# Performance work log

Measured on AMD Instinct MI355X. Metric: run time of the kernel, lower is better.

Reference implementation:

```python
import jax, jax.numpy as jnp
import numpy as np

B, N, D, H = 2, 64, 256, 8
DK = D // H
EPS = 1e-5


def layer_norm(x, g, b):
    mu = jnp.mean(x, axis=-1, keepdims=True)
    var = jnp.var(x, axis=-1, keepdims=True)
    return (x - mu) * jax.lax.rsqrt(var + EPS) * g + b


def setup_inputs() -> dict:
    key = jax.random.key(0)
    ks = jax.random.split(key, 12)
    s = 1.0 / np.sqrt(D)
    inp = {
        "x": jax.random.normal(ks[0], (B, N, N, D), jnp.float32),
        "W_lk": jax.random.uniform(ks[1], (D, D), jnp.float32, -s, s),
        "W_rk": jax.random.uniform(ks[2], (D, D), jnp.float32, -s, s),
        "W_lv": jax.random.uniform(ks[3], (D, D), jnp.float32, -s, s),
        "W_rv": jax.random.uniform(ks[4], (D, D), jnp.float32, -s, s),
        "W_out": jax.random.uniform(ks[5], (D, D), jnp.float32, -s, s),
        "ln_agg_g": jnp.ones((D,), jnp.float32),
        "ln_agg_b": jnp.zeros((D,), jnp.float32),
        "W1": jax.random.uniform(ks[6], (D, 2 * D), jnp.float32, -s, s),
        "b1": jnp.zeros((2 * D,), jnp.float32),
        "W2": jax.random.uniform(ks[7], (2 * D, D), jnp.float32, -1.0 / np.sqrt(2 * D), 1.0 / np.sqrt(2 * D)),
        "b2": jnp.zeros((D,), jnp.float32),
        "ln2_g": jnp.ones((D,), jnp.float32),
        "ln2_b": jnp.zeros((D,), jnp.float32),
    }
    return inp


def reference(x, W_lk, W_rk, W_lv, W_rv, W_out, ln_agg_g, ln_agg_b, W1, b1, W2, b2, ln2_g, ln2_b):
    b, n = x.shape[0], x.shape[1]
    # projections (no bias), split into heads: [b, n, n, H, DK]
    lk = (x @ W_lk).reshape(b, n, n, H, DK)
    rk = (x @ W_rk).reshape(b, n, n, H, DK)
    lv = (x @ W_lv).reshape(b, n, n, H, DK)
    rv = (x @ W_rv).reshape(b, n, n, H, DK)
    # triangle attention scores over intermediate node 'a'
    scores = jnp.einsum('bxahd,bayhd->bxayh', lk, rk) / np.sqrt(DK)
    att = jax.nn.softmax(scores, axis=2)
    # fused triangle value aggregation: sum_a att * lv[x,a] * rv[a,y]
    o = jnp.einsum('bxayh,bxahd,bayhd->bxyhd', att, lv, rv)
    o = o.reshape(b, n, n, D) @ W_out
    # FFN block (dropout = 0)
    h = layer_norm(x + o, ln_agg_g, ln_agg_b)
    m = jax.nn.relu(h @ W1 + b1) @ W2 + b2
    return layer_norm(m + h, ln2_g, ln2_b)
```

## Files before the change

kernel.cpp:

```cpp
#include <hip/hip_runtime.h>

#define ROWS 8192
#define DIM  256

typedef short short8 __attribute__((ext_vector_type(8)));
typedef float f4     __attribute__((ext_vector_type(4)));

__device__ __forceinline__ float bf2f(unsigned int u16) {
    union { unsigned int i; float f; } v;
    v.i = (u16 & 0xffffu) << 16;
    return v.f;
}
__device__ __forceinline__ unsigned short f2bf(float f) {
    union { float f; unsigned int u; } v; v.f = f;
    unsigned int r = v.u + 0x7fffu + ((v.u >> 16) & 1u);
    return (unsigned short)(r >> 16);
}

__global__ __launch_bounds__(256)
void cast_all(const float* __restrict__ x, unsigned short* __restrict__ xb,
              const float* __restrict__ w0, const float* __restrict__ w1,
              const float* __restrict__ w2, const float* __restrict__ w3,
              const float* __restrict__ w4, const float* __restrict__ w5,
              const float* __restrict__ w6, unsigned short* __restrict__ wt)
{
    if (blockIdx.x < 2048) {
        const size_t i = ((size_t)blockIdx.x * 256 + threadIdx.x) * 4;
        float4 v = *(const float4*)(x + i);
        uint2 p;
        p.x = f2bf(v.x) | ((unsigned int)f2bf(v.y) << 16);
        p.y = f2bf(v.z) | ((unsigned int)f2bf(v.w) << 16);
        *(uint2*)(xb + i) = p;
        return;
    }
    __shared__ float t[32][33];
    int id = blockIdx.x - 2048;
    const float* src; int K, N, Ntiles; size_t doff;
    if (id < 320) {
        int w = id >> 6; id &= 63; K = 256; N = 256; Ntiles = 8;
        doff = (size_t)w * 65536;
        src = (w == 0) ? w0 : (w == 1) ? w1 : (w == 2) ? w2 : (w == 3) ? w3 : w4;
    } else if (id < 448) {
        id -= 320; K = 256; N = 512; Ntiles = 16; doff = 327680; src = w5;
    } else {
        id -= 448; K = 512; N = 256; Ntiles = 8;  doff = 458752; src = w6;
    }
    const int tk = id / Ntiles, tn = id % Ntiles;
    const int k0 = tk * 32, n0 = tn * 32;
    const int c = threadIdx.x & 31, r8 = threadIdx.x >> 5;
    for (int rr = r8; rr < 32; rr += 8)
        t[rr][c] = src[(size_t)(k0 + rr) * N + n0 + c];
    __syncthreads();
    for (int rr = r8; rr < 32; rr += 8)
        wt[doff + (size_t)(n0 + rr) * K + k0 + c] = f2bf(t[c][rr]);
}

__global__ __launch_bounds__(256)
void proj_mfma(const unsigned short* __restrict__ A, const unsigned short* __restrict__ WT,
               unsigned short* __restrict__ projT)
{
    const int lane = threadIdx.x & 63, wave = threadIdx.x >> 6;
    const int wsel = blockIdx.x >> 2;
    const int col0 = (blockIdx.x & 3) * 64;
    const int m0 = blockIdx.y * 128 + wave * 32;
    const int lm = lane & 15, lk8 = (lane >> 4) * 8;
    const unsigned short* W = WT + (size_t)wsel * 65536;
    unsigned short* dst = projT + (size_t)wsel * 2097152;

    f4 acc[2][4];
    #pragma unroll
    for (int i = 0; i < 2; ++i)
        #pragma unroll
        for (int j = 0; j < 4; ++j) acc[i][j] = (f4){0.f, 0.f, 0.f, 0.f};

    #pragma unroll 2
    for (int kc = 0; kc < 256; kc += 32) {
        short8 af[2], bf[4];
        #pragma unroll
        for (int i = 0; i < 2; ++i)
            af[i] = *(const short8*)(A + (size_t)(m0 + i * 16 + lm) * 256 + kc + lk8);
        #pragma unroll
        for (int j = 0; j < 4; ++j)
            bf[j] = *(const short8*)(W + (size_t)(col0 + j * 16 + lm) * 256 + kc + lk8);
        #pragma unroll
        for (int i = 0; i < 2; ++i)
            #pragma unroll
            for (int j = 0; j < 4; ++j)
                acc[i][j] = __builtin_amdgcn_mfma_f32_16x16x32_bf16(af[i], bf[j], acc[i][j], 0, 0, 0);
    }

    const int rbase = (lane >> 4) * 4;
    const int swap = (wsel == 3);
    #pragma unroll
    for (int i = 0; i < 2; ++i)
        #pragma unroll
        for (int j = 0; j < 4; ++j) {
            const int c = col0 + j * 16 + lm;
            const int h = c >> 5, d = c & 31;
            #pragma unroll
            for (int r = 0; r < 4; ++r) {
                const int m = m0 + i * 16 + rbase + r;
                const int b = m >> 12, ii = (m >> 6) & 63, jj = m & 63;
                const int p = swap ? jj : ii;
                const int q = swap ? ii : jj;
                const size_t idx = ((((size_t)b * 8 + h) * 64 + p) * 64 + q) * 32 + d;
                dst[idx] = f2bf(acc[i][j][r]);
            }
        }
}

__global__ __launch_bounds__(256)
void scores_mfma(const unsigned short* __restrict__ lkT, const unsigned short* __restrict__ rkT,
                 unsigned short* __restrict__ S)
{
    const int lane = threadIdx.x & 63, wave = threadIdx.x >> 6;
    const int bi = blockIdx.x;
    const int b = bi >> 7, h = (bi >> 4) & 7, a = (bi & 15) * 4 + wave;
    const size_t bh = (size_t)b * 8 + h;
    const int lm = lane & 15, lk8 = (lane >> 4) * 8;

    short8 af[4], bf[4];
    #pragma unroll
    for (int t = 0; t < 4; ++t) {
        af[t] = *(const short8*)(lkT + ((bh * 64 + (t * 16 + lm)) * 64 + a) * 32 + lk8);
        bf[t] = *(const short8*)(rkT + ((bh * 64 + a) * 64 + (t * 16 + lm)) * 32 + lk8);
    }
    const int rbase = (lane >> 4) * 4;
    unsigned short* Sb = S + bh * 262144 + a * 64;
    #pragma unroll
    for (int mt = 0; mt < 4; ++mt)
        #pragma unroll
        for (int nt = 0; nt < 4; ++nt) {
            f4 acc = (f4){0.f, 0.f, 0.f, 0.f};
            acc = __builtin_amdgcn_mfma_f32_16x16x32_bf16(af[mt], bf[nt], acc, 0, 0, 0);
            #pragma unroll
            for (int r = 0; r < 4; ++r) {
                const int xx = mt * 16 + rbase + r;
                const int yy = nt * 16 + lm;
                Sb[(size_t)xx * 4096 + yy] = f2bf(acc[r] * 0.17677669529663687f);
            }
        }
}

__global__ __launch_bounds__(256)
void softmax_agg(const unsigned short* __restrict__ S, const unsigned short* __restrict__ lvT,
                 const unsigned short* __restrict__ rvT, unsigned short* __restrict__ obuf)
{
    __shared__ float att[64][64];
    __shared__ float lvL[64][32];
    __shared__ float smx[4][64], ssm[4][64], invL[64];
    const int bi = blockIdx.x;
    const int b = bi >> 9, h = (bi >> 6) & 7, x = bi & 63;
    const size_t bh = (size_t)b * 8 + h;
    const int tid = threadIdx.x;

    {
        const int a = tid >> 2, yo = (tid & 3) * 16;
        const unsigned short* Sp = S + (bh * 64 + x) * 4096 + a * 64 + yo;
        uint4 p0 = *(const uint4*)(Sp);
        uint4 p1 = *(const uint4*)(Sp + 8);
        att[a][yo +  0] = bf2f(p0.x); att[a][yo +  1] = bf2f(p0.x >> 16);
        att[a][yo +  2] = bf2f(p0.y); att[a][yo +  3] = bf2f(p0.y >> 16);
        att[a][yo +  4] = bf2f(p0.z); att[a][yo +  5] = bf2f(p0.z >> 16);
        att[a][yo +  6] = bf2f(p0.w); att[a][yo +  7] = bf2f(p0.w >> 16);
        att[a][yo +  8] = bf2f(p1.x); att[a][yo +  9] = bf2f(p1.x >> 16);
        att[a][yo + 10] = bf2f(p1.y); att[a][yo + 11] = bf2f(p1.y >> 16);
        att[a][yo + 12] = bf2f(p1.z); att[a][yo + 13] = bf2f(p1.z >> 16);
        att[a][yo + 14] = bf2f(p1.w); att[a][yo + 15] = bf2f(p1.w >> 16);
        const int d0 = (tid & 3) * 8;
        uint4 q = *(const uint4*)(lvT + ((bh * 64 + x) * 64 + a) * 32 + d0);
        lvL[a][d0 + 0] = bf2f(q.x); lvL[a][d0 + 1] = bf2f(q.x >> 16);
        lvL[a][d0 + 2] = bf2f(q.y); lvL[a][d0 + 3] = bf2f(q.y >> 16);
        lvL[a][d0 + 4] = bf2f(q.z); lvL[a][d0 + 5] = bf2f(q.z >> 16);
        lvL[a][d0 + 6] = bf2f(q.w); lvL[a][d0 + 7] = bf2f(q.w >> 16);
    }
    __syncthreads();

    {
        const int y = tid & 63, az = tid >> 6;
        float mx = -1e30f;
        for (int a = az; a < 64; a += 4) mx = fmaxf(mx, att[a][y]);
        smx[az][y] = mx;
    }
    __syncthreads();

    {
        const int y = tid & 63, az = tid >> 6;
        const float mx = fmaxf(fmaxf(smx[0][y], smx[1][y]), fmaxf(smx[2][y], smx[3][y]));
        float s = 0.f;
        for (int a = az; a < 64; a += 4) {
            float e = __expf(att[a][y] - mx);
            att[a][y] = e;
            s += e;
        }
        ssm[az][y] = s;
    }
    __syncthreads();
    if (tid < 64)
        invL[tid] = 1.f / (ssm[0][tid] + ssm[1][tid] + ssm[2][tid] + ssm[3][tid]);
    __syncthreads();

    {
        const int y = tid >> 2, d0 = (tid & 3) * 8;
        float o[8];
        #pragma unroll
        for (int i = 0; i < 8; ++i) o[i] = 0.f;
        const unsigned short* rvr = rvT + (bh * 64 + y) * 2048 + d0;
        #pragma unroll 8
        for (int a = 0; a < 64; ++a) {
            const float w = att[a][y];
            float4 lv0 = *(const float4*)&lvL[a][d0];
            float4 lv1 = *(const float4*)&lvL[a][d0 + 4];
            uint4 rv4 = *(const uint4*)(rvr + (size_t)a * 32);
            o[0] = fmaf(w * lv0.x, bf2f(rv4.x),       o[0]);
            o[1] = fmaf(w * lv0.y, bf2f(rv4.x >> 16), o[1]);
            o[2] = fmaf(w * lv0.z, bf2f(rv4.y),       o[2]);
            o[3] = fmaf(w * lv0.w, bf2f(rv4.y >> 16), o[3]);
            o[4] = fmaf(w * lv1.x, bf2f(rv4.z),       o[4]);
            o[5] = fmaf(w * lv1.y, bf2f(rv4.z >> 16), o[5]);
            o[6] = fmaf(w * lv1.z, bf2f(rv4.w),       o[6]);
            o[7] = fmaf(w * lv1.w, bf2f(rv4.w >> 16), o[7]);
        }
        const float inv = invL[y];
        uint4 pk;
        pk.x = f2bf(o[0] * inv) | ((unsigned int)f2bf(o[1] * inv) << 16);
        pk.y = f2bf(o[2] * inv) | ((unsigned int)f2bf(o[3] * inv) << 16);
        pk.z = f2bf(o[4] * inv) | ((unsigned int)f2bf(o[5] * inv) << 16);
        pk.w = f2bf(o[6] * inv) | ((unsigned int)f2bf(o[7] * inv) << 16);
        *(uint4*)(obuf + (((size_t)b * 64 + x) * 64 + y) * 256 + h * 32 + d0) = pk;
    }
}

__global__ __launch_bounds__(256)
void gemm_ln1(const unsigned short* __restrict__ A, const unsigned short* __restrict__ WT,
              const float* __restrict__ resid,
              const float* __restrict__ gamma, const float* __restrict__ beta,
              unsigned short* __restrict__ out)
{
    constexpr int K = 256;
    __shared__ float ps[16][4], pq[16][4];
    const int lane = threadIdx.x & 63, wave = threadIdx.x >> 6;
    const int m0 = blockIdx.x * 16;
    const int col0 = wave * 64;
    const int lm = lane & 15, lk8 = (lane >> 4) * 8;

    f4 acc[4];
    #pragma unroll
    for (int j = 0; j < 4; ++j) acc[j] = (f4){0.f, 0.f, 0.f, 0.f};

    #pragma unroll 2
    for (int kc = 0; kc < K; kc += 32) {
        short8 af = *(const short8*)(A + (size_t)(m0 + lm) * K + kc + lk8);
        #pragma unroll
        for (int j = 0; j < 4; ++j) {
            short8 bf = *(const short8*)(WT + (size_t)(col0 + j * 16 + lm) * K + kc + lk8);
            acc[j] = __builtin_amdgcn_mfma_f32_16x16x32_bf16(af, bf, acc[j], 0, 0, 0);
        }
    }

    const int rbase = (lane >> 4) * 4;
    float v[4][4];
    float s[4] = {0.f, 0.f, 0.f, 0.f}, q[4] = {0.f, 0.f, 0.f, 0.f};
    #pragma unroll
    for (int j = 0; j < 4; ++j) {
        const int n = col0 + j * 16 + lm;
        #pragma unroll
        for (int r = 0; r < 4; ++r) {
            const int m = m0 + rbase + r;
            float t = acc[j][r] + resid[(size_t)m * 256 + n];
            v[j][r] = t;
            s[r] += t;
            q[r] = fmaf(t, t, q[r]);
        }
    }
    #pragma unroll
    for (int off = 1; off < 16; off <<= 1) {
        #pragma unroll
        for (int r = 0; r < 4; ++r) {
            s[r] += __shfl_xor(s[r], off);
            q[r] += __shfl_xor(q[r], off);
        }
    }
    if (lm == 0) {
        #pragma unroll
        for (int r = 0; r < 4; ++r) {
            ps[rbase + r][wave] = s[r];
            pq[rbase + r][wave] = q[r];
        }
    }
    __syncthreads();
    #pragma unroll
    for (int r = 0; r < 4; ++r) {
        const int lr = rbase + r;
        const float Sm = ps[lr][0] + ps[lr][1] + ps[lr][2] + ps[lr][3];
        const float Qm = pq[lr][0] + pq[lr][1] + pq[lr][2] + pq[lr][3];
        const float mu = Sm * (1.f / 256.f);
        const float ri = rsqrtf(Qm * (1.f / 256.f) - mu * mu + 1e-5f);
        const int m = m0 + lr;
        #pragma unroll
        for (int j = 0; j < 4; ++j) {
            const int n = col0 + j * 16 + lm;
            out[(size_t)m * 256 + n] = f2bf((v[j][r] - mu) * ri * gamma[n] + beta[n]);
        }
    }
}

__global__ __launch_bounds__(256)
void ffn_fused(const unsigned short* __restrict__ hb, const unsigned short* __restrict__ WT1,
               const float* __restrict__ b1, const unsigned short* __restrict__ WT2,
               const float* __restrict__ b2, const float* __restrict__ gamma,
               const float* __restrict__ beta, float* __restrict__ out)
{
    __shared__ unsigned short mid[16][520];
    __shared__ float ps[16][4], pq[16][4];
    const int lane = threadIdx.x & 63, wave = threadIdx.x >> 6;
    const int m0 = blockIdx.x * 16;
    const int lm = lane & 15, lk8 = (lane >> 4) * 8;
    const int rbase = (lane >> 4) * 4;

    short8 af[8];
    #pragma unroll
    for (int kc = 0; kc < 8; ++kc)
        af[kc] = *(const short8*)(hb + (size_t)(m0 + lm) * 256 + kc * 32 + lk8);
    const int colb = wave * 128;
    #pragma unroll
    for (int j = 0; j < 8; ++j) {
        const int n = colb + j * 16 + lm;
        f4 acc = (f4){0.f, 0.f, 0.f, 0.f};
        #pragma unroll
        for (int kc = 0; kc < 8; ++kc) {
            short8 bf = *(const short8*)(WT1 + (size_t)n * 256 + kc * 32 + lk8);
            acc = __builtin_amdgcn_mfma_f32_16x16x32_bf16(af[kc], bf, acc, 0, 0, 0);
        }
        const float bb = b1[n];
        #pragma unroll
        for (int r = 0; r < 4; ++r)
            mid[rbase + r][n] = f2bf(fmaxf(acc[r] + bb, 0.f));
    }
    __syncthreads();

    const int col0 = wave * 64;
    f4 acc2[4];
    #pragma unroll
    for (int j = 0; j < 4; ++j) acc2[j] = (f4){0.f, 0.f, 0.f, 0.f};
    #pragma unroll 4
    for (int kc = 0; kc < 16; ++kc) {
        short8 a2 = *(const short8*)&mid[lm][kc * 32 + lk8];
        #pragma unroll
        for (int j = 0; j < 4; ++j) {
            short8 bf = *(const short8*)(WT2 + (size_t)(col0 + j * 16 + lm) * 512 + kc * 32 + lk8);
            acc2[j] = __builtin_amdgcn_mfma_f32_16x16x32_bf16(a2, bf, acc2[j], 0, 0, 0);
        }
    }

    float v[4][4];
    float s[4] = {0.f, 0.f, 0.f, 0.f}, q[4] = {0.f, 0.f, 0.f, 0.f};
    #pragma unroll
    for (int j = 0; j < 4; ++j) {
        const int n = col0 + j * 16 + lm;
        const float bb = b2[n];
        #pragma unroll
        for (int r = 0; r < 4; ++r) {
            const int m = m0 + rbase + r;
            float t = acc2[j][r] + bb + bf2f(hb[(size_t)m * 256 + n]);
            v[j][r] = t;
            s[r] += t;
            q[r] = fmaf(t, t, q[r]);
        }
    }
    #pragma unroll
    for (int off = 1; off < 16; off <<= 1) {
        #pragma unroll
        for (int r = 0; r < 4; ++r) {
            s[r] += __shfl_xor(s[r], off);
            q[r] += __shfl_xor(q[r], off);
        }
    }
    if (lm == 0) {
        #pragma unroll
        for (int r = 0; r < 4; ++r) {
            ps[rbase + r][wave] = s[r];
            pq[rbase + r][wave] = q[r];
        }
    }
    __syncthreads();
    #pragma unroll
    for (int r = 0; r < 4; ++r) {
        const int lr = rbase + r;
        const float Sm = ps[lr][0] + ps[lr][1] + ps[lr][2] + ps[lr][3];
        const float Qm = pq[lr][0] + pq[lr][1] + pq[lr][2] + pq[lr][3];
        const float mu = Sm * (1.f / 256.f);
        const float ri = rsqrtf(Qm * (1.f / 256.f) - mu * mu + 1e-5f);
        const int m = m0 + lr;
        #pragma unroll
        for (int j = 0; j < 4; ++j) {
            const int n = col0 + j * 16 + lm;
            out[(size_t)m * 256 + n] = (v[j][r] - mu) * ri * gamma[n] + beta[n];
        }
    }
}

extern "C" void kernel_launch(void* const* d_in, const int* in_sizes, int n_in,
                              void* d_out, int out_size, void* d_ws, size_t ws_size,
                              hipStream_t stream)
{
    const float* x    = (const float*)d_in[0];
    const float* Wlk  = (const float*)d_in[1];
    const float* Wrk  = (const float*)d_in[2];
    const float* Wlv  = (const float*)d_in[3];
    const float* Wrv  = (const float*)d_in[4];
    const float* Wout = (const float*)d_in[5];
    const float* g1   = (const float*)d_in[6];
    const float* be1  = (const float*)d_in[7];
    const float* W1   = (const float*)d_in[8];
    const float* b1   = (const float*)d_in[9];
    const float* W2   = (const float*)d_in[10];
    const float* b2   = (const float*)d_in[11];
    const float* g2   = (const float*)d_in[12];
    const float* be2  = (const float*)d_in[13];

    char* base = (char*)d_ws;
    const size_t MB = 1ull << 20;
    unsigned short* xb    = (unsigned short*)(base + 0);
    unsigned short* obufb = (unsigned short*)(base + 0);
    unsigned short* projT = (unsigned short*)(base + 4 * MB);
    unsigned short* lkT   = projT;
    unsigned short* rkT   = projT + 2097152;
    unsigned short* lvT   = projT + 2 * 2097152;
    unsigned short* rvT   = projT + 3 * 2097152;
    unsigned short* hb    = (unsigned short*)(base + 20 * MB);
    unsigned short* Sbuf  = (unsigned short*)(base + 32 * MB);
    unsigned short* WT    = (unsigned short*)(base + 40 * MB);

    cast_all<<<2624, 256, 0, stream>>>(x, xb, Wlk, Wrk, Wlv, Wrv, Wout, W1, W2, WT);
    proj_mfma<<<dim3(16, 64), 256, 0, stream>>>(xb, WT, projT);
    scores_mfma<<<256, 256, 0, stream>>>(lkT, rkT, Sbuf);
    softmax_agg<<<1024, 256, 0, stream>>>(Sbuf, lvT, rvT, obufb);
    gemm_ln1<<<512, 256, 0, stream>>>(obufb, WT + 262144, x, g1, be1, hb);
    ffn_fused<<<512, 256, 0, stream>>>(hb, WT + 327680, b1, WT + 458752, b2, g2, be2, (float*)d_out);
}
```

Measured before the change: 189.7 us.

## Split fused FFN into tiled GEMM kernels and halve scores work per wave

The fused FFN kernel, which kept the ReLU intermediate in shared memory per 16-row block, is split into two kernels. The first is a 2D-tiled GEMM (128x64 tiles) that writes the bf16 intermediate to global memory. The second is a GEMM that applies the second linear layer, adds the residual and applies layer norm. The scores kernel now gives each wave half the x-rows and launches twice as many blocks, for more parallelism. The split is meant to improve weight reuse and occupancy, at the cost of an extra 8 MB global round trip and one more launch.

Measured after the change: 192.8 us. Within noise of the previous version (+1.7%).

```diff
diff --git a/kernel.cpp b/kernel.cpp
--- a/kernel.cpp
+++ b/kernel.cpp
@@ -115,27 +115,30 @@
 {
     const int lane = threadIdx.x & 63, wave = threadIdx.x >> 6;
     const int bi = blockIdx.x;
-    const int b = bi >> 7, h = (bi >> 4) & 7, a = (bi & 15) * 4 + wave;
-    const size_t bh = (size_t)b * 8 + h;
+    const size_t bh = bi >> 5;
+    const int s = (bi & 31) * 4 + wave;
+    const int a = s >> 1, half = s & 1;
     const int lm = lane & 15, lk8 = (lane >> 4) * 8;
 
-    short8 af[4], bf[4];
-    #pragma unroll
-    for (int t = 0; t < 4; ++t) {
-        af[t] = *(const short8*)(lkT + ((bh * 64 + (t * 16 + lm)) * 64 + a) * 32 + lk8);
+    short8 af[2], bf[4];
+    #pragma unroll
+    for (int t = 0; t < 2; ++t)
+        af[t] = *(const short8*)(lkT + ((bh * 64 + ((half * 2 + t) * 16 + lm)) * 64 + a) * 32 + lk8);
+    #pragma unroll
+    for (int t = 0; t < 4; ++t)
         bf[t] = *(const short8*)(rkT + ((bh * 64 + a) * 64 + (t * 16 + lm)) * 32 + lk8);
-    }
+
     const int rbase = (lane >> 4) * 4;
     unsigned short* Sb = S + bh * 262144 + a * 64;
     #pragma unroll
-    for (int mt = 0; mt < 4; ++mt)
+    for (int mt = 0; mt < 2; ++mt)
         #pragma unroll
         for (int nt = 0; nt < 4; ++nt) {
             f4 acc = (f4){0.f, 0.f, 0.f, 0.f};
             acc = __builtin_amdgcn_mfma_f32_16x16x32_bf16(af[mt], bf[nt], acc, 0, 0, 0);
             #pragma unroll
             for (int r = 0; r < 4; ++r) {
-                const int xx = mt * 16 + rbase + r;
+                const int xx = (half * 2 + mt) * 16 + rbase + r;
                 const int yy = nt * 16 + lm;
                 Sb[(size_t)xx * 4096 + yy] = f2bf(acc[r] * 0.17677669529663687f);
             }
@@ -306,63 +309,90 @@
 }
 
 __global__ __launch_bounds__(256)
-void ffn_fused(const unsigned short* __restrict__ hb, const unsigned short* __restrict__ WT1,
-               const float* __restrict__ b1, const unsigned short* __restrict__ WT2,
-               const float* __restrict__ b2, const float* __restrict__ gamma,
-               const float* __restrict__ beta, float* __restrict__ out)
-{
-    __shared__ unsigned short mid[16][520];
+void gemm_ffn1(const unsigned short* __restrict__ A, const unsigned short* __restrict__ WT,
+               const float* __restrict__ bias, unsigned short* __restrict__ outB)
+{
+    constexpr int K = 256, N = 512;
+    const int lane = threadIdx.x & 63, wave = threadIdx.x >> 6;
+    const int m0 = blockIdx.y * 128 + wave * 32;
+    const int col0 = blockIdx.x * 64;
+    const int lm = lane & 15, lk8 = (lane >> 4) * 8;
+
+    f4 acc[2][4];
+    #pragma unroll
+    for (int i = 0; i < 2; ++i)
+        #pragma unroll
+        for (int j = 0; j < 4; ++j) acc[i][j] = (f4){0.f, 0.f, 0.f, 0.f};
+
+    #pragma unroll 2
+    for (int kc = 0; kc < K; kc += 32) {
+        short8 af[2], bf[4];
+        #pragma unroll
+        for (int i = 0; i < 2; ++i)
+            af[i] = *(const short8*)(A + (size_t)(m0 + i * 16 + lm) * K + kc + lk8);
+        #pragma unroll
+        for (int j = 0; j < 4; ++j)
+            bf[j] = *(const short8*)(WT + (size_t)(col0 + j * 16 + lm) * K + kc + lk8);
+        #pragma unroll
+        for (int i = 0; i < 2; ++i)
+            #pragma unroll
+            for (int j = 0; j < 4; ++j)
+                acc[i][j] = __builtin_amdgcn_mfma_f32_16x16x32_bf16(af[i], bf[j], acc[i][j], 0, 0, 0);
+    }
+
+    const int rbase = (lane >> 4) * 4;
+    #pragma unroll
+    for (int i = 0; i < 2; ++i)
+        #pragma unroll
+        for (int j = 0; j < 4; ++j) {
+            const int n = col0 + j * 16 + lm;
+            const float bb = bias[n];
+            #pragma unroll
+            for (int r = 0; r < 4; ++r) {
+                const int m = m0 + i * 16 + rbase + r;
+                outB[(size_t)m * N + n] = f2bf(fmaxf(acc[i][j][r] + bb, 0.f));
+            }
+        }
+}
+
+__global__ __launch_bounds__(256)
+void gemm_ln2(const unsigned short* __restrict__ A, const unsigned short* __restrict__ WT,
+              const float* __restrict__ bias, const unsigned short* __restrict__ resid,
+              const float* __restrict__ gamma, const float* __restrict__ beta,
+              float* __restrict__ out)
+{
+    constexpr int K = 512;
     __shared__ float ps[16][4], pq[16][4];
     const int lane = threadIdx.x & 63, wave = threadIdx.x >> 6;
     const int m0 = blockIdx.x * 16;
+    const int col0 = wave * 64;
     const int lm = lane & 15, lk8 = (lane >> 4) * 8;
+
+    f4 acc[4];
+    #pragma unroll
+    for (int j = 0; j < 4; ++j) acc[j] = (f4){0.f, 0.f, 0.f, 0.f};
+
+    #pragma unroll 2
+    for (int kc = 0; kc < K; kc += 32) {
+        short8 af = *(const short8*)(A + (size_t)(m0 + lm) * K + kc + lk8);
+        #pragma unroll
+        for (int j = 0; j < 4; ++j) {
+            short8 bf = *(const short8*)(WT + (size_t)(col0 + j * 16 + lm) * K + kc + lk8);
+            acc[j] = __builtin_amdgcn_mfma_f32_16x16x32_bf16(af, bf, acc[j], 0, 0, 0);
+        }
+    }
+
     const int rbase = (lane >> 4) * 4;
-
-    short8 af[8];
-    #pragma unroll
-    for (int kc = 0; kc < 8; ++kc)
-        af[kc] = *(const short8*)(hb + (size_t)(m0 + lm) * 256 + kc * 32 + lk8);
-    const int colb = wave * 128;
-    #pragma unroll
-    for (int j = 0; j < 8; ++j) {
-        const int n = colb + j * 16 + lm;
-        f4 acc = (f4){0.f, 0.f, 0.f, 0.f};
-        #pragma unroll
-        for (int kc = 0; kc < 8; ++kc) {
-            short8 bf = *(const short8*)(WT1 + (size_t)n * 256 + kc * 32 + lk8);
-            acc = __builtin_amdgcn_mfma_f32_16x16x32_bf16(af[kc], bf, acc, 0, 0, 0);
-        }
-        const float bb = b1[n];
-        #pragma unroll
-        for (int r = 0; r < 4; ++r)
-            mid[rbase + r][n] = f2bf(fmaxf(acc[r] + bb, 0.f));
-    }
-    __syncthreads();
-
-    const int col0 = wave * 64;
-    f4 acc2[4];
-    #pragma unroll
-    for (int j = 0; j < 4; ++j) acc2[j] = (f4){0.f, 0.f, 0.f, 0.f};
-    #pragma unroll 4
-    for (int kc = 0; kc < 16; ++kc) {
-        short8 a2 = *(const short8*)&mid[lm][kc * 32 + lk8];
-        #pragma unroll
-        for (int j = 0; j < 4; ++j) {
-            short8 bf = *(const short8*)(WT2 + (size_t)(col0 + j * 16 + lm) * 512 + kc * 32 + lk8);
-            acc2[j] = __builtin_amdgcn_mfma_f32_16x16x32_bf16(a2, bf, acc2[j], 0, 0, 0);
-        }
-    }
-
     float v[4][4];
     float s[4] = {0.f, 0.f, 0.f, 0.f}, q[4] = {0.f, 0.f, 0.f, 0.f};
     #pragma unroll
     for (int j = 0; j < 4; ++j) {
         const int n = col0 + j * 16 + lm;
-        const float bb = b2[n];
+        const float bb = bias[n];
         #pragma unroll
         for (int r = 0; r < 4; ++r) {
             const int m = m0 + rbase + r;
-            float t = acc2[j][r] + bb + bf2f(hb[(size_t)m * 256 + n]);
+            float t = acc[j][r] + bb + bf2f(resid[(size_t)m * 256 + n]);
             v[j][r] = t;
             s[r] += t;
             q[r] = fmaf(t, t, q[r]);
@@ -429,13 +459,15 @@
     unsigned short* lvT   = projT + 2 * 2097152;
     unsigned short* rvT   = projT + 3 * 2097152;
     unsigned short* hb    = (unsigned short*)(base + 20 * MB);
+    unsigned short* midb  = (unsigned short*)(base + 24 * MB);
     unsigned short* Sbuf  = (unsigned short*)(base + 32 * MB);
     unsigned short* WT    = (unsigned short*)(base + 40 * MB);
 
     cast_all<<<2624, 256, 0, stream>>>(x, xb, Wlk, Wrk, Wlv, Wrv, Wout, W1, W2, WT);
     proj_mfma<<<dim3(16, 64), 256, 0, stream>>>(xb, WT, projT);
-    scores_mfma<<<256, 256, 0, stream>>>(lkT, rkT, Sbuf);
+    scores_mfma<<<512, 256, 0, stream>>>(lkT, rkT, Sbuf);
     softmax_agg<<<1024, 256, 0, stream>>>(Sbuf, lvT, rvT, obufb);
     gemm_ln1<<<512, 256, 0, stream>>>(obufb, WT + 262144, x, g1, be1, hb);
-    ffn_fused<<<512, 256, 0, stream>>>(hb, WT + 327680, b1, WT + 458752, b2, g2, be2, (float*)d_out);
-}
+    gemm_ffn1<<<dim3(8, 64), 256, 0, stream>>>(hb, WT + 327680, b1, midb);
+    gemm_ln2<<<512, 256, 0, stream>>>(midb, WT + 458752, b2, hb, g2, be2, (float*)d_out);
+}
```
